# Performance work log

Measured on AMD Instinct MI355X. Metric: run time of the kernel, lower is better.

The kernel has to match this reference:

```python
import math
import jax, jax.numpy as jnp
import numpy as np

L, H, W_SIZE, EPS = 4, 4, 64, 1e-5


def _sinusoidal_pe(T, D):
    pos = np.arange(T, dtype=np.float32)[:, None]
    div = np.exp(np.arange(0, D, 2, dtype=np.float32) * -(math.log(10000.0) / D))
    pe = np.zeros((T, D), dtype=np.float32)
    pe[:, 0::2] = np.sin(pos * div)
    pe[:, 1::2] = np.cos(pos * div)
    return jnp.asarray(pe)


def _layernorm(x, g, b):
    mu = jnp.mean(x, axis=-1, keepdims=True)
    var = jnp.mean(jnp.square(x - mu), axis=-1, keepdims=True)
    return (x - mu) * jax.lax.rsqrt(var + EPS) * g + b


def setup_inputs() -> dict:
    key = jax.random.key(0)
    B, T, D, F = 4, 2048, 256, 1024
    ks = jax.random.split(key, 8)
    s = 0.02
    return {
        "tokens": jax.random.normal(ks[0], (B, T, D), jnp.float32),
        "Wqkv": jax.random.normal(ks[1], (L, 3 * D, D), jnp.float32) * s,
        "bqkv": jnp.zeros((L, 3 * D), jnp.float32),
        "Wo": jax.random.normal(ks[2], (L, D, D), jnp.float32) * s,
        "bo": jnp.zeros((L, D), jnp.float32),
        "W1": jax.random.normal(ks[3], (L, F, D), jnp.float32) * s,
        "b1": jnp.zeros((L, F), jnp.float32),
        "W2": jax.random.normal(ks[4], (L, D, F), jnp.float32) * s,
        "b2": jnp.zeros((L, D), jnp.float32),
        "ln1_g": jnp.ones((L, D), jnp.float32),
        "ln1_b": jnp.zeros((L, D), jnp.float32),
        "ln2_g": jnp.ones((L, D), jnp.float32),
        "ln2_b": jnp.zeros((L, D), jnp.float32),
        "lnf_g": jnp.ones((D,), jnp.float32),
        "lnf_b": jnp.zeros((D,), jnp.float32),
    }


def reference(tokens, Wqkv, bqkv, Wo, bo, W1, b1, W2, b2,
              ln1_g, ln1_b, ln2_g, ln2_b, lnf_g, lnf_b):
    B, T, D = tokens.shape
    hd = D // H
    x = tokens + _sinusoidal_pe(T, D)[None]  # (B,T,D)

    # sliding-window causal mask: i attends to max(0, i-W+1)..i
    idx = jnp.arange(T)
    i, j = idx[:, None], idx[None, :]
    allowed = (j <= i) & (j >= i - W_SIZE + 1)
    bias = jnp.where(allowed, 0.0, -1e9).astype(jnp.float32)  # (T,T)

    def step(x, p):
        Wqkv, bqkv, Wo, bo, W1, b1, W2, b2, g1, be1, g2, be2 = p
        x2 = _layernorm(x, g1, be1)
        qkv = x2 @ Wqkv.T + bqkv                      # (B,T,3D)
        q, k, v = jnp.split(qkv, 3, axis=-1)
        q = q.reshape(B, T, H, hd)
        k = k.reshape(B, T, H, hd)
        v = v.reshape(B, T, H, hd)
        scores = jnp.einsum("bthd,bshd->bhts", q, k) / math.sqrt(hd)
        attn = jax.nn.softmax(scores + bias, axis=-1)
        o = jnp.einsum("bhts,bshd->bthd", attn, v).reshape(B, T, D)
        x = x + o @ Wo.T + bo
        x3 = _layernorm(x, g2, be2)
        h = jax.nn.gelu(x3 @ W1.T + b1, approximate=False)
        x = x + h @ W2.T + b2
        return x, None

    x, _ = jax.lax.scan(step, x, (Wqkv, bqkv, Wo, bo, W1, b1, W2, b2,
                                  ln1_g, ln1_b, ln2_g, ln2_b))
    return _layernorm(x, lnf_g, lnf_b)
```

## Files before the change

### kernel.cpp

```cpp
#include <hip/hip_runtime.h>
#include <hip/hip_bf16.h>
#include <math.h>

#define BB 4
#define TT 2048
#define DD 256
#define FF 1024
#define NL 4

typedef __bf16 bf16x8 __attribute__((ext_vector_type(8)));
typedef float f32x4 __attribute__((ext_vector_type(4)));

__device__ __forceinline__ float gelu_f(float v) {
  float x = fabsf(v) * 0.70710678118654752f;
  float t = 1.0f / fmaf(0.3275911f, x, 1.0f);
  float p = t * fmaf(t, fmaf(t, fmaf(t, fmaf(t, 1.061405429f, -1.453152027f),
                                     1.421413741f), -0.284496736f), 0.254829592f);
  float erfv = copysignf(1.0f - p * __expf(-x * x), v);
  return 0.5f * v * (1.0f + erfv);
}

__global__ __launch_bounds__(256) void prologue_kernel(
    const float4* __restrict__ wq, const float4* __restrict__ wo,
    const float4* __restrict__ w1, const float4* __restrict__ w2,
    ushort4* __restrict__ dst,
    const float* __restrict__ tokens, const float* __restrict__ g,
    const float* __restrict__ b, float* __restrict__ x,
    __hip_bfloat16* __restrict__ sb) {
  if (blockIdx.x < 3072) {
    int gi = blockIdx.x * 256 + threadIdx.x;
    const float4* src;
    int off;
    if (gi < 196608)      { src = wq; off = gi; }
    else if (gi < 262144) { src = wo; off = gi - 196608; }
    else if (gi < 524288) { src = w1; off = gi - 262144; }
    else                  { src = w2; off = gi - 524288; }
    float4 v = src[off];
    ushort4 o;
    o.x = __hip_bfloat16_raw(__float2bfloat16(v.x)).x;
    o.y = __hip_bfloat16_raw(__float2bfloat16(v.y)).x;
    o.z = __hip_bfloat16_raw(__float2bfloat16(v.z)).x;
    o.w = __hip_bfloat16_raw(__float2bfloat16(v.w)).x;
    dst[gi] = o;
    return;
  }
  int row = (blockIdx.x - 3072) * 4 + (threadIdx.x >> 6);
  int lane = threadIdx.x & 63;
  int t = row & (TT - 1);
  const float* xr = tokens + (size_t)row * DD;
  float v[4];
  float s = 0.f;
#pragma unroll
  for (int i = 0; i < 4; ++i) {
    int d = lane + 64 * i;
    int i2 = d & ~1;
    float freq = expf((float)i2 * -(9.210340371976184f / 256.f));
    float ang = (float)t * freq;
    float pe = (d & 1) ? cosf(ang) : sinf(ang);
    v[i] = xr[d] + pe;
    s += v[i];
  }
#pragma unroll
  for (int off = 32; off; off >>= 1) s += __shfl_xor(s, off, 64);
  float mu = s * (1.f / DD);
  float vs = 0.f;
#pragma unroll
  for (int i = 0; i < 4; ++i) { float dd = v[i] - mu; vs = fmaf(dd, dd, vs); }
#pragma unroll
  for (int off = 32; off; off >>= 1) vs += __shfl_xor(vs, off, 64);
  float rr = rsqrtf(vs * (1.f / DD) + 1e-5f);
#pragma unroll
  for (int i = 0; i < 4; ++i) {
    int d = lane + 64 * i;
    x[(size_t)row * DD + d] = v[i];
    sb[(size_t)row * DD + d] = __float2bfloat16((v[i] - mu) * rr * g[d] + b[d]);
  }
}

template <int MW, int NW, int BK, int KTOT, int ACT>
__global__ __launch_bounds__(256) void mgemm_kernel(
    const __hip_bfloat16* __restrict__ A, const __hip_bfloat16* __restrict__ B,
    const float* __restrict__ bias, __hip_bfloat16* __restrict__ Cout,
    int M, int N) {
  constexpr int BM = 32 * MW, BN = 32 * NW, ROWS = BM + BN;
  constexpr int NCH = BK / 32;
  constexpr int CHB = ROWS * 32;
  constexpr int RG = ROWS / 16;
  constexpr int NST = NCH * RG;
  __shared__ __align__(16) __hip_bfloat16 sm[NCH * CHB];
  const int tid = threadIdx.x;
  const int wave = tid >> 6, lane = tid & 63;
  const int m0 = blockIdx.y * BM, n0 = blockIdx.x * BN;
  const int wm = (wave >> 1) * (16 * MW), wn = (wave & 1) * (16 * NW);
  const int quad = lane >> 4, lr = lane & 15;
  const int srow = lane >> 2, scol = (lane & 3) * 8;

  f32x4 acc[MW][NW] = {};

  for (int kt = 0; kt < KTOT; kt += BK) {
    __syncthreads();
#pragma unroll
    for (int i = 0; i < NST / 4; ++i) {
      int inst = i * 4 + wave;
      int c = inst / RG, grp = inst - c * RG;
      int r = grp * 16 + srow;
      const __hip_bfloat16* gp =
          (r < BM) ? (A + (size_t)(m0 + r) * KTOT + kt + c * 32 + scol)
                   : (B + (size_t)(n0 + (r - BM)) * KTOT + kt + c * 32 + scol);
      __builtin_amdgcn_global_load_lds(
          (const __attribute__((address_space(1))) unsigned int*)gp,
          (__attribute__((address_space(3))) unsigned int*)(sm + c * CHB + grp * 512),
          16, 0, 0);
    }
    __syncthreads();
#pragma unroll
    for (int c = 0; c < NCH; ++c) {
      bf16x8 af[MW], bfr[NW];
#pragma unroll
      for (int mi = 0; mi < MW; ++mi)
        af[mi] = *(const bf16x8*)(sm + c * CHB + (wm + mi * 16 + lr) * 32 + quad * 8);
#pragma unroll
      for (int ni = 0; ni < NW; ++ni)
        bfr[ni] = *(const bf16x8*)(sm + c * CHB + (BM + wn + ni * 16 + lr) * 32 + quad * 8);
#pragma unroll
      for (int mi = 0; mi < MW; ++mi)
#pragma unroll
        for (int ni = 0; ni < NW; ++ni)
          acc[mi][ni] = __builtin_amdgcn_mfma_f32_16x16x32_bf16(
              af[mi], bfr[ni], acc[mi][ni], 0, 0, 0);
    }
  }

#pragma unroll
  for (int mi = 0; mi < MW; ++mi) {
#pragma unroll
    for (int ni = 0; ni < NW; ++ni) {
      int col = n0 + wn + ni * 16 + lr;
      float bv = bias[col];
#pragma unroll
      for (int r = 0; r < 4; ++r) {
        int row = m0 + wm + mi * 16 + quad * 4 + r;
        float v = acc[mi][ni][r] + bv;
        if (ACT == 1) v = gelu_f(v);
        Cout[(size_t)row * N + col] = __float2bfloat16(v);
      }
    }
  }
}

template <int KTOT, int FIN>
__global__ __launch_bounds__(256) void mgemm_ln_kernel(
    const __hip_bfloat16* __restrict__ A, const __hip_bfloat16* __restrict__ B,
    const float* __restrict__ bias, const float* __restrict__ res,
    const float* __restrict__ g, const float* __restrict__ bb,
    float* __restrict__ xout, void* __restrict__ yout) {
  constexpr int BM = 32, ROWS = BM + 256;
  constexpr int BK = 64, NCH = BK / 32;
  constexpr int CHB = ROWS * 32;
  constexpr int RG = ROWS / 16;
  constexpr int NST = NCH * RG;
  __shared__ __align__(16) __hip_bfloat16 sm[NCH * CHB];
  __shared__ float red1[4][BM], red2[4][BM];
  const int tid = threadIdx.x;
  const int wave = tid >> 6, lane = tid & 63;
  const int quad = lane >> 4, lr = lane & 15;
  const int m0 = blockIdx.x * BM;
  const int srow = lane >> 2, scol = (lane & 3) * 8;

  f32x4 acc[2][4] = {};

  for (int kt = 0; kt < KTOT; kt += BK) {
    __syncthreads();
#pragma unroll
    for (int i = 0; i < NST / 4; ++i) {
      int inst = i * 4 + wave;
      int c = inst / RG, grp = inst - c * RG;
      int r = grp * 16 + srow;
      const __hip_bfloat16* gp =
          (r < BM) ? (A + (size_t)(m0 + r) * KTOT + kt + c * 32 + scol)
                   : (B + (size_t)(r - BM) * KTOT + kt + c * 32 + scol);
      __builtin_amdgcn_global_load_lds(
          (const __attribute__((address_space(1))) unsigned int*)gp,
          (__attribute__((address_space(3))) unsigned int*)(sm + c * CHB + grp * 512),
          16, 0, 0);
    }
    __syncthreads();
#pragma unroll
    for (int c = 0; c < NCH; ++c) {
      bf16x8 af[2], bfr[4];
#pragma unroll
      for (int mi = 0; mi < 2; ++mi)
        af[mi] = *(const bf16x8*)(sm + c * CHB + (mi * 16 + lr) * 32 + quad * 8);
#pragma unroll
      for (int ni = 0; ni < 4; ++ni)
        bfr[ni] = *(const bf16x8*)(sm + c * CHB + (BM + wave * 64 + ni * 16 + lr) * 32 + quad * 8);
#pragma unroll
      for (int mi = 0; mi < 2; ++mi)
#pragma unroll
        for (int ni = 0; ni < 4; ++ni)
          acc[mi][ni] = __builtin_amdgcn_mfma_f32_16x16x32_bf16(
              af[mi], bfr[ni], acc[mi][ni], 0, 0, 0);
    }
  }

  float v[2][4][4];
  float s1[2][4] = {}, s2[2][4] = {};
#pragma unroll
  for (int mi = 0; mi < 2; ++mi)
#pragma unroll
    for (int ni = 0; ni < 4; ++ni) {
      int col = wave * 64 + ni * 16 + lr;
      float bv = bias[col];
#pragma unroll
      for (int r = 0; r < 4; ++r) {
        int row = m0 + mi * 16 + quad * 4 + r;
        float val = acc[mi][ni][r] + bv + res[(size_t)row * DD + col];
        v[mi][ni][r] = val;
        s1[mi][r] += val;
        s2[mi][r] = fmaf(val, val, s2[mi][r]);
      }
    }
#pragma unroll
  for (int mi = 0; mi < 2; ++mi)
#pragma unroll
    for (int r = 0; r < 4; ++r) {
#pragma unroll
      for (int off = 8; off; off >>= 1) {
        s1[mi][r] += __shfl_xor(s1[mi][r], off, 64);
        s2[mi][r] += __shfl_xor(s2[mi][r], off, 64);
      }
    }
  if (lr == 0) {
#pragma unroll
    for (int mi = 0; mi < 2; ++mi)
#pragma unroll
      for (int r = 0; r < 4; ++r) {
        red1[wave][mi * 16 + quad * 4 + r] = s1[mi][r];
        red2[wave][mi * 16 + quad * 4 + r] = s2[mi][r];
      }
  }
  __syncthreads();
#pragma unroll
  for (int mi = 0; mi < 2; ++mi)
#pragma unroll
    for (int r = 0; r < 4; ++r) {
      int rl = mi * 16 + quad * 4 + r;
      float ssum = red1[0][rl] + red1[1][rl] + red1[2][rl] + red1[3][rl];
      float qsum = red2[0][rl] + red2[1][rl] + red2[2][rl] + red2[3][rl];
      float mu = ssum * (1.f / DD);
      float var = qsum * (1.f / DD) - mu * mu;
      float rr = rsqrtf(var + 1e-5f);
      int row = m0 + rl;
#pragma unroll
      for (int ni = 0; ni < 4; ++ni) {
        int col = wave * 64 + ni * 16 + lr;
        float y = (v[mi][ni][r] - mu) * rr * g[col] + bb[col];
        if (FIN) {
          ((float*)yout)[(size_t)row * DD + col] = y;
        } else {
          ((__hip_bfloat16*)yout)[(size_t)row * DD + col] = __float2bfloat16(y);
          xout[(size_t)row * DD + col] = v[mi][ni][r];
        }
      }
    }
}

__global__ __launch_bounds__(256) void attn_kernel(const __hip_bfloat16* __restrict__ qkv,
                                                   __hip_bfloat16* __restrict__ o) {
  __shared__ __align__(16) __hip_bfloat16 KsPs[128 * 72];
  __shared__ __align__(16) __hip_bfloat16 Vt[64 * 136];
  const int bh = blockIdx.y;
  const int b = bh >> 2, h = bh & 3;
  const int t0 = blockIdx.x * 64;
  const int sbase = t0 - 63;
  const int tid = threadIdx.x;

  const __hip_bfloat16* kb = qkv + (size_t)(b * TT) * 768 + 256 + h * 64;
  const __hip_bfloat16* vb = kb + 256;
  union U8 { uint4 u; __hip_bfloat16 hx[8]; };
#pragma unroll
  for (int it = 0; it < 4; ++it) {
    int f = tid + it * 256;
    int si = f >> 3;
    int c8 = f & 7;
    int s = sbase + si;
    U8 kr, vr;
    kr.u = make_uint4(0, 0, 0, 0); vr.u = make_uint4(0, 0, 0, 0);
    if (s >= 0 && s < TT) {
      kr.u = *(const uint4*)&kb[(size_t)s * 768 + 8 * c8];
      vr.u = *(const uint4*)&vb[(size_t)s * 768 + 8 * c8];
    }
    *(uint4*)&KsPs[si * 72 + c8 * 8] = kr.u;
    int pc = (si >> 3) ^ c8;
#pragma unroll
    for (int j = 0; j < 8; ++j) Vt[(c8 * 8 + j) * 136 + pc * 8 + (si & 7)] = vr.hx[j];
  }
  __syncthreads();

  const int wave = tid >> 6, lane = tid & 63;
  const int quad = lane >> 4, lr = lane & 15;

  const __hip_bfloat16* qrow = qkv + (size_t)(b * TT + t0 + wave * 16 + lr) * 768 + h * 64;
  bf16x8 qa0 = *(const bf16x8*)(qrow + quad * 8);
  bf16x8 qa1 = *(const bf16x8*)(qrow + 32 + quad * 8);
  f32x4 sc[8];
#pragma unroll
  for (int c = 0; c < 8; ++c) {
    f32x4 a = {};
    bf16x8 kf0 = *(const bf16x8*)&KsPs[(c * 16 + lr) * 72 + quad * 8];
    a = __builtin_amdgcn_mfma_f32_16x16x32_bf16(qa0, kf0, a, 0, 0, 0);
    bf16x8 kf1 = *(const bf16x8*)&KsPs[(c * 16 + lr) * 72 + 32 + quad * 8];
    a = __builtin_amdgcn_mfma_f32_16x16x32_bf16(qa1, kf1, a, 0, 0, 0);
    sc[c] = a;
  }
  __syncthreads();

#pragma unroll
  for (int reg = 0; reg < 4; ++reg) {
    int dt = wave * 16 + quad * 4 + reg;
    float pv[8];
    float mx = -1e30f;
#pragma unroll
    for (int c = 0; c < 8; ++c) {
      int si = c * 16 + lr;
      float v = sc[c][reg] * 0.125f;
      bool ok = (si >= dt) && (si <= dt + 63) && (sbase + si >= 0);
      v = ok ? v : -1e30f;
      pv[c] = v;
      mx = fmaxf(mx, v);
    }
#pragma unroll
    for (int off = 8; off; off >>= 1) mx = fmaxf(mx, __shfl_xor(mx, off, 64));
    float l = 0.f;
#pragma unroll
    for (int c = 0; c < 8; ++c) { float e = __expf(pv[c] - mx); pv[c] = e; l += e; }
#pragma unroll
    for (int off = 8; off; off >>= 1) l += __shfl_xor(l, off, 64);
    float rinv = 1.f / l;
#pragma unroll
    for (int c = 0; c < 8; ++c)
      KsPs[(wave * 16 + quad * 4 + reg) * 136 + c * 16 + lr] = __float2bfloat16(pv[c] * rinv);
  }

  __hip_bfloat16* obase = o + (size_t)(b * TT) * DD + h * 64;
#pragma unroll
  for (int ct = 0; ct < 4; ++ct) {
    f32x4 acc = {};
#pragma unroll
    for (int kk = 0; kk < 4; ++kk) {
      bf16x8 pa = *(const bf16x8*)&KsPs[(wave * 16 + lr) * 136 + kk * 32 + quad * 8];
      int dd = ct * 16 + lr;
      bf16x8 vf = *(const bf16x8*)&Vt[dd * 136 + (((kk * 4 + quad) ^ (dd >> 3)) * 8)];
      acc = __builtin_amdgcn_mfma_f32_16x16x32_bf16(pa, vf, acc, 0, 0, 0);
    }
#pragma unroll
    for (int reg = 0; reg < 4; ++reg) {
      int t = t0 + wave * 16 + quad * 4 + reg;
      obase[(size_t)t * DD + ct * 16 + lr] = __float2bfloat16(acc[reg]);
    }
  }
}

extern "C" void kernel_launch(void* const* d_in, const int* in_sizes, int n_in,
                              void* d_out, int out_size, void* d_ws, size_t ws_size,
                              hipStream_t stream) {
  const float* tokens = (const float*)d_in[0];
  const float* Wqkv = (const float*)d_in[1];
  const float* bqkv = (const float*)d_in[2];
  const float* Wo   = (const float*)d_in[3];
  const float* bo   = (const float*)d_in[4];
  const float* W1   = (const float*)d_in[5];
  const float* b1   = (const float*)d_in[6];
  const float* W2   = (const float*)d_in[7];
  const float* b2   = (const float*)d_in[8];
  const float* ln1g = (const float*)d_in[9];
  const float* ln1b = (const float*)d_in[10];
  const float* ln2g = (const float*)d_in[11];
  const float* ln2b = (const float*)d_in[12];
  const float* lnfg = (const float*)d_in[13];
  const float* lnfb = (const float*)d_in[14];
  float* out = (float*)d_out;

  const int M = BB * TT;
  const int ND = M * DD;

  float* x = (float*)d_ws;
  __hip_bfloat16* sb  = (__hip_bfloat16*)(x + ND);
  __hip_bfloat16* big = sb + (size_t)M * DD;
  __hip_bfloat16* wqb = big + (size_t)M * FF;
  __hip_bfloat16* wob = wqb + (size_t)NL * 3 * DD * DD;
  __hip_bfloat16* w1b = wob + (size_t)NL * DD * DD;
  __hip_bfloat16* w2b = w1b + (size_t)NL * FF * DD;

  prologue_kernel<<<3072 + M / 4, 256, 0, stream>>>(
      (const float4*)Wqkv, (const float4*)Wo, (const float4*)W1,
      (const float4*)W2, (ushort4*)wqb, tokens, ln1g, ln1b, x, sb);

  for (int l = 0; l < NL; ++l) {
    mgemm_kernel<2, 4, 64, 256, 0><<<dim3(6, 128), 256, 0, stream>>>(
        sb, wqb + (size_t)l * 768 * DD, bqkv + l * 768, big, M, 768);
    attn_kernel<<<dim3(TT / 64, BB * 4), 256, 0, stream>>>(big, sb);
    mgemm_ln_kernel<256, 0><<<M / 32, 256, 0, stream>>>(
        sb, wob + (size_t)l * DD * DD, bo + l * DD, x,
        ln2g + l * DD, ln2b + l * DD, x, sb);
    mgemm_kernel<2, 4, 64, 256, 1><<<dim3(8, 128), 256, 0, stream>>>(
        sb, w1b + (size_t)l * FF * DD, b1 + l * FF, big, M, FF);
    if (l < NL - 1) {
      mgemm_ln_kernel<1024, 0><<<M / 32, 256, 0, stream>>>(
          big, w2b + (size_t)l * DD * FF, b2 + l * DD, x,
          ln1g + (l + 1) * DD, ln1b + (l + 1) * DD, x, sb);
    } else {
      mgemm_ln_kernel<1024, 1><<<M / 32, 256, 0, stream>>>(
          big, w2b + (size_t)l * DD * FF, b2 + l * DD, x,
          lnfg, lnfb, nullptr, out);
    }
  }
}
```

Measured before the change: 371.7 us.

## Fuse FFN up/down projections, LayerNorm and next-layer QKV GEMM into one kernel

Adds an mlp_kernel in which each 32-row block computes W1+GELU in 128-wide chunks held in LDS, accumulates the W2 projection, applies residual plus LayerNorm, and then runs the next layer's QKV projection from LDS. This removes the round trip of the (M,1024) hidden activation through global memory and two kernel launches per layer. In exchange each block re-streams all weights with no cross-block reuse, using only 256 blocks with large LDS (~84KB). Occupancy is low and there is no double buffering.

Result: slower. 397.5 us (+6.9%).

```diff
diff --git a/kernel.cpp b/kernel.cpp
--- a/kernel.cpp
+++ b/kernel.cpp
@@ -10,6 +10,12 @@
 
 typedef __bf16 bf16x8 __attribute__((ext_vector_type(8)));
 typedef float f32x4 __attribute__((ext_vector_type(4)));
+
+__device__ __forceinline__ void stage16(const __hip_bfloat16* gp, __hip_bfloat16* lp) {
+  __builtin_amdgcn_global_load_lds(
+      (const __attribute__((address_space(1))) unsigned int*)gp,
+      (__attribute__((address_space(3))) unsigned int*)lp, 16, 0, 0);
+}
 
 __device__ __forceinline__ float gelu_f(float v) {
   float x = fabsf(v) * 0.70710678118654752f;
@@ -107,10 +113,7 @@
       const __hip_bfloat16* gp =
           (r < BM) ? (A + (size_t)(m0 + r) * KTOT + kt + c * 32 + scol)
                    : (B + (size_t)(n0 + (r - BM)) * KTOT + kt + c * 32 + scol);
-      __builtin_amdgcn_global_load_lds(
-          (const __attribute__((address_space(1))) unsigned int*)gp,
-          (__attribute__((address_space(3))) unsigned int*)(sm + c * CHB + grp * 512),
-          16, 0, 0);
+      stage16(gp, sm + c * CHB + grp * 512);
     }
     __syncthreads();
 #pragma unroll
@@ -179,10 +182,7 @@
       const __hip_bfloat16* gp =
           (r < BM) ? (A + (size_t)(m0 + r) * KTOT + kt + c * 32 + scol)
                    : (B + (size_t)(r - BM) * KTOT + kt + c * 32 + scol);
-      __builtin_amdgcn_global_load_lds(
-          (const __attribute__((address_space(1))) unsigned int*)gp,
-          (__attribute__((address_space(3))) unsigned int*)(sm + c * CHB + grp * 512),
-          16, 0, 0);
+      stage16(gp, sm + c * CHB + grp * 512);
     }
     __syncthreads();
 #pragma unroll
@@ -263,6 +263,221 @@
         }
       }
     }
+}
+
+template <int LAST>
+__global__ __launch_bounds__(256) void mlp_kernel(
+    const __hip_bfloat16* __restrict__ sb, const __hip_bfloat16* __restrict__ w1,
+    const float* __restrict__ b1, const __hip_bfloat16* __restrict__ w2,
+    const float* __restrict__ b2, const __hip_bfloat16* __restrict__ wq,
+    const float* __restrict__ bq, const float* __restrict__ g,
+    const float* __restrict__ bb, float* __restrict__ x,
+    __hip_bfloat16* __restrict__ big, float* __restrict__ out) {
+  __shared__ __align__(16) __hip_bfloat16 asbuf[8 * 1024];
+  __shared__ __align__(16) __hip_bfloat16 sbuf2[8 * 1024];
+  __shared__ __align__(16) __hip_bfloat16 hbuf[32 * 136];
+  __shared__ __align__(16) __hip_bfloat16 wstage[16384];
+  __shared__ float red1[4][32], red2[4][32];
+  const int tid = threadIdx.x;
+  const int wave = tid >> 6, lane = tid & 63;
+  const int quad = lane >> 4, lr = lane & 15;
+  const int srow = lane >> 2, scol = (lane & 3) * 8;
+  const int t0 = blockIdx.x * 32;
+
+#pragma unroll
+  for (int i = 0; i < 4; ++i) {
+    int inst = i * 4 + wave;
+    int c = inst >> 1, grp = inst & 1;
+    int r = grp * 16 + srow;
+    stage16(sb + (size_t)(t0 + r) * 256 + c * 32 + scol,
+            asbuf + c * 1024 + grp * 512);
+  }
+  __syncthreads();
+
+  f32x4 xacc[2][4] = {};
+  for (int fc = 0; fc < 8; ++fc) {
+    const int ff0 = fc * 128;
+    f32x4 hacc[2][2] = {};
+#pragma unroll
+    for (int kt2 = 0; kt2 < 2; ++kt2) {
+      __syncthreads();
+#pragma unroll
+      for (int i = 0; i < 8; ++i) {
+        int inst = i * 4 + wave;
+        int c2 = inst >> 3, grp = inst & 7;
+        int r = grp * 16 + srow;
+        stage16(w1 + (size_t)(ff0 + r) * 256 + kt2 * 128 + c2 * 32 + scol,
+                wstage + c2 * 4096 + grp * 512);
+      }
+      __syncthreads();
+#pragma unroll
+      for (int c2 = 0; c2 < 4; ++c2) {
+        bf16x8 af[2], bfr[2];
+#pragma unroll
+        for (int mi = 0; mi < 2; ++mi)
+          af[mi] = *(const bf16x8*)(asbuf + (kt2 * 4 + c2) * 1024 + (mi * 16 + lr) * 32 + quad * 8);
+#pragma unroll
+        for (int ni = 0; ni < 2; ++ni)
+          bfr[ni] = *(const bf16x8*)(wstage + c2 * 4096 + (wave * 2 + ni) * 512 + lr * 32 + quad * 8);
+#pragma unroll
+        for (int mi = 0; mi < 2; ++mi)
+#pragma unroll
+          for (int ni = 0; ni < 2; ++ni)
+            hacc[mi][ni] = __builtin_amdgcn_mfma_f32_16x16x32_bf16(
+                af[mi], bfr[ni], hacc[mi][ni], 0, 0, 0);
+      }
+    }
+#pragma unroll
+    for (int mi = 0; mi < 2; ++mi)
+#pragma unroll
+      for (int ni = 0; ni < 2; ++ni) {
+        int col = wave * 32 + ni * 16 + lr;
+        float bv = b1[ff0 + col];
+#pragma unroll
+        for (int r = 0; r < 4; ++r)
+          hbuf[(mi * 16 + quad * 4 + r) * 136 + col] =
+              __float2bfloat16(gelu_f(hacc[mi][ni][r] + bv));
+      }
+    __syncthreads();
+#pragma unroll
+    for (int kt3 = 0; kt3 < 2; ++kt3) {
+      if (kt3) __syncthreads();
+#pragma unroll
+      for (int i = 0; i < 8; ++i) {
+        int inst = i * 4 + wave;
+        int c2 = inst >> 4, grp = inst & 15;
+        int r = grp * 16 + srow;
+        stage16(w2 + (size_t)r * 1024 + ff0 + kt3 * 64 + c2 * 32 + scol,
+                wstage + c2 * 8192 + grp * 512);
+      }
+      __syncthreads();
+#pragma unroll
+      for (int c2 = 0; c2 < 2; ++c2) {
+        bf16x8 af[2], bfr[4];
+#pragma unroll
+        for (int mi = 0; mi < 2; ++mi)
+          af[mi] = *(const bf16x8*)(hbuf + (mi * 16 + lr) * 136 + kt3 * 64 + c2 * 32 + quad * 8);
+#pragma unroll
+        for (int ni = 0; ni < 4; ++ni)
+          bfr[ni] = *(const bf16x8*)(wstage + c2 * 8192 + (wave * 4 + ni) * 512 + lr * 32 + quad * 8);
+#pragma unroll
+        for (int mi = 0; mi < 2; ++mi)
+#pragma unroll
+          for (int ni = 0; ni < 4; ++ni)
+            xacc[mi][ni] = __builtin_amdgcn_mfma_f32_16x16x32_bf16(
+                af[mi], bfr[ni], xacc[mi][ni], 0, 0, 0);
+      }
+    }
+  }
+
+  float v[2][4][4];
+  float s1[2][4] = {}, s2[2][4] = {};
+#pragma unroll
+  for (int mi = 0; mi < 2; ++mi)
+#pragma unroll
+    for (int ni = 0; ni < 4; ++ni) {
+      int col = wave * 64 + ni * 16 + lr;
+      float bv = b2[col];
+#pragma unroll
+      for (int r = 0; r < 4; ++r) {
+        int row = t0 + mi * 16 + quad * 4 + r;
+        float val = xacc[mi][ni][r] + bv + x[(size_t)row * DD + col];
+        v[mi][ni][r] = val;
+        s1[mi][r] += val;
+        s2[mi][r] = fmaf(val, val, s2[mi][r]);
+      }
+    }
+#pragma unroll
+  for (int mi = 0; mi < 2; ++mi)
+#pragma unroll
+    for (int r = 0; r < 4; ++r) {
+#pragma unroll
+      for (int off = 8; off; off >>= 1) {
+        s1[mi][r] += __shfl_xor(s1[mi][r], off, 64);
+        s2[mi][r] += __shfl_xor(s2[mi][r], off, 64);
+      }
+    }
+  if (lr == 0) {
+#pragma unroll
+    for (int mi = 0; mi < 2; ++mi)
+#pragma unroll
+      for (int r = 0; r < 4; ++r) {
+        red1[wave][mi * 16 + quad * 4 + r] = s1[mi][r];
+        red2[wave][mi * 16 + quad * 4 + r] = s2[mi][r];
+      }
+  }
+  __syncthreads();
+#pragma unroll
+  for (int mi = 0; mi < 2; ++mi)
+#pragma unroll
+    for (int r = 0; r < 4; ++r) {
+      int rl = mi * 16 + quad * 4 + r;
+      float ssum = red1[0][rl] + red1[1][rl] + red1[2][rl] + red1[3][rl];
+      float qsum = red2[0][rl] + red2[1][rl] + red2[2][rl] + red2[3][rl];
+      float mu = ssum * (1.f / DD);
+      float var = qsum * (1.f / DD) - mu * mu;
+      float rr = rsqrtf(var + 1e-5f);
+      int row = t0 + rl;
+#pragma unroll
+      for (int ni = 0; ni < 4; ++ni) {
+        int col = wave * 64 + ni * 16 + lr;
+        float y = (v[mi][ni][r] - mu) * rr * g[col] + bb[col];
+        if (LAST) {
+          out[(size_t)row * DD + col] = y;
+        } else {
+          x[(size_t)row * DD + col] = v[mi][ni][r];
+          sbuf2[(col >> 5) * 1024 + rl * 32 + (col & 31)] = __float2bfloat16(y);
+        }
+      }
+    }
+
+  if (!LAST) {
+    __syncthreads();
+    for (int nc = 0; nc < 6; ++nc) {
+      f32x4 qacc[2][2] = {};
+#pragma unroll
+      for (int kt2 = 0; kt2 < 2; ++kt2) {
+        __syncthreads();
+#pragma unroll
+        for (int i = 0; i < 8; ++i) {
+          int inst = i * 4 + wave;
+          int c2 = inst >> 3, grp = inst & 7;
+          int r = grp * 16 + srow;
+          stage16(wq + (size_t)(nc * 128 + r) * 256 + kt2 * 128 + c2 * 32 + scol,
+                  wstage + c2 * 4096 + grp * 512);
+        }
+        __syncthreads();
+#pragma unroll
+        for (int c2 = 0; c2 < 4; ++c2) {
+          bf16x8 af[2], bfr[2];
+#pragma unroll
+          for (int mi = 0; mi < 2; ++mi)
+            af[mi] = *(const bf16x8*)(sbuf2 + (kt2 * 4 + c2) * 1024 + (mi * 16 + lr) * 32 + quad * 8);
+#pragma unroll
+          for (int ni = 0; ni < 2; ++ni)
+            bfr[ni] = *(const bf16x8*)(wstage + c2 * 4096 + (wave * 2 + ni) * 512 + lr * 32 + quad * 8);
+#pragma unroll
+          for (int mi = 0; mi < 2; ++mi)
+#pragma unroll
+            for (int ni = 0; ni < 2; ++ni)
+              qacc[mi][ni] = __builtin_amdgcn_mfma_f32_16x16x32_bf16(
+                  af[mi], bfr[ni], qacc[mi][ni], 0, 0, 0);
+        }
+      }
+#pragma unroll
+      for (int mi = 0; mi < 2; ++mi)
+#pragma unroll
+        for (int ni = 0; ni < 2; ++ni) {
+          int col = nc * 128 + wave * 32 + ni * 16 + lr;
+          float bv = bq[col];
+#pragma unroll
+          for (int r = 0; r < 4; ++r) {
+            int row = t0 + mi * 16 + quad * 4 + r;
+            big[(size_t)row * 768 + col] = __float2bfloat16(qacc[mi][ni][r] + bv);
+          }
+        }
+    }
+  }
 }
 
 __global__ __launch_bounds__(256) void attn_kernel(const __hip_bfloat16* __restrict__ qkv,
@@ -396,23 +611,25 @@
       (const float4*)Wqkv, (const float4*)Wo, (const float4*)W1,
       (const float4*)W2, (ushort4*)wqb, tokens, ln1g, ln1b, x, sb);
 
+  mgemm_kernel<2, 4, 64, 256, 0><<<dim3(6, 128), 256, 0, stream>>>(
+      sb, wqb, bqkv, big, M, 768);
+
   for (int l = 0; l < NL; ++l) {
-    mgemm_kernel<2, 4, 64, 256, 0><<<dim3(6, 128), 256, 0, stream>>>(
-        sb, wqb + (size_t)l * 768 * DD, bqkv + l * 768, big, M, 768);
     attn_kernel<<<dim3(TT / 64, BB * 4), 256, 0, stream>>>(big, sb);
     mgemm_ln_kernel<256, 0><<<M / 32, 256, 0, stream>>>(
         sb, wob + (size_t)l * DD * DD, bo + l * DD, x,
         ln2g + l * DD, ln2b + l * DD, x, sb);
-    mgemm_kernel<2, 4, 64, 256, 1><<<dim3(8, 128), 256, 0, stream>>>(
-        sb, w1b + (size_t)l * FF * DD, b1 + l * FF, big, M, FF);
     if (l < NL - 1) {
-      mgemm_ln_kernel<1024, 0><<<M / 32, 256, 0, stream>>>(
-          big, w2b + (size_t)l * DD * FF, b2 + l * DD, x,
-          ln1g + (l + 1) * DD, ln1b + (l + 1) * DD, x, sb);
+      mlp_kernel<0><<<M / 32, 256, 0, stream>>>(
+          sb, w1b + (size_t)l * FF * DD, b1 + l * FF,
+          w2b + (size_t)l * DD * FF, b2 + l * DD,
+          wqb + (size_t)(l + 1) * 768 * DD, bqkv + (l + 1) * 768,
+          ln1g + (l + 1) * DD, ln1b + (l + 1) * DD, x, big, nullptr);
     } else {
-      mgemm_ln_kernel<1024, 1><<<M / 32, 256, 0, stream>>>(
-          big, w2b + (size_t)l * DD * FF, b2 + l * DD, x,
-          lnfg, lnfb, nullptr, out);
-    }
-  }
-}
+      mlp_kernel<1><<<M / 32, 256, 0, stream>>>(
+          sb, w1b + (size_t)l * FF * DD, b1 + l * FF,
+          w2b + (size_t)l * DD * FF, b2 + l * DD,
+          nullptr, nullptr, lnfg, lnfb, x, nullptr, out);
+    }
+  }
+}
```

## Split W2 GEMM from fused residual-LayerNorm into tiled GEMM plus row-LN kernel

Applied to the files above, without the earlier changes.

The FFN down-projection (K=1024) no longer uses the fused GEMM+LayerNorm kernel with 32-row blocks spanning all 256 columns. It now runs as a regular tiled GEMM with 64x64 tiles and fp32 output into a new workspace buffer, followed by a separate residual-add plus LayerNorm kernel. This gives 512 blocks instead of 256 and smaller per-block B tiles, which is meant to improve occupancy and load balance for the heaviest GEMM. The cost is an extra fp32 round trip through global memory and one more launch per layer. The QKV GEMM launch is also reordered so it follows the new LN kernel.

New measurement: 361.1 us. 2.8% less time.

```diff
diff --git a/kernel.cpp b/kernel.cpp
--- a/kernel.cpp
+++ b/kernel.cpp
@@ -10,6 +10,12 @@
 
 typedef __bf16 bf16x8 __attribute__((ext_vector_type(8)));
 typedef float f32x4 __attribute__((ext_vector_type(4)));
+
+__device__ __forceinline__ void stage16(const __hip_bfloat16* gp, __hip_bfloat16* lp) {
+  __builtin_amdgcn_global_load_lds(
+      (const __attribute__((address_space(1))) unsigned int*)gp,
+      (__attribute__((address_space(3))) unsigned int*)lp, 16, 0, 0);
+}
 
 __device__ __forceinline__ float gelu_f(float v) {
   float x = fabsf(v) * 0.70710678118654752f;
@@ -77,10 +83,10 @@
   }
 }
 
-template <int MW, int NW, int BK, int KTOT, int ACT>
+template <int MW, int NW, int BK, int KTOT, int ACT, int OUTF>
 __global__ __launch_bounds__(256) void mgemm_kernel(
     const __hip_bfloat16* __restrict__ A, const __hip_bfloat16* __restrict__ B,
-    const float* __restrict__ bias, __hip_bfloat16* __restrict__ Cout,
+    const float* __restrict__ bias, void* __restrict__ Cout,
     int M, int N) {
   constexpr int BM = 32 * MW, BN = 32 * NW, ROWS = BM + BN;
   constexpr int NCH = BK / 32;
@@ -107,10 +113,7 @@
       const __hip_bfloat16* gp =
           (r < BM) ? (A + (size_t)(m0 + r) * KTOT + kt + c * 32 + scol)
                    : (B + (size_t)(n0 + (r - BM)) * KTOT + kt + c * 32 + scol);
-      __builtin_amdgcn_global_load_lds(
-          (const __attribute__((address_space(1))) unsigned int*)gp,
-          (__attribute__((address_space(3))) unsigned int*)(sm + c * CHB + grp * 512),
-          16, 0, 0);
+      stage16(gp, sm + c * CHB + grp * 512);
     }
     __syncthreads();
 #pragma unroll
@@ -142,18 +145,19 @@
         int row = m0 + wm + mi * 16 + quad * 4 + r;
         float v = acc[mi][ni][r] + bv;
         if (ACT == 1) v = gelu_f(v);
-        Cout[(size_t)row * N + col] = __float2bfloat16(v);
+        if (OUTF) ((float*)Cout)[(size_t)row * N + col] = v;
+        else ((__hip_bfloat16*)Cout)[(size_t)row * N + col] = __float2bfloat16(v);
       }
     }
   }
 }
 
-template <int KTOT, int FIN>
+template <int KTOT>
 __global__ __launch_bounds__(256) void mgemm_ln_kernel(
     const __hip_bfloat16* __restrict__ A, const __hip_bfloat16* __restrict__ B,
     const float* __restrict__ bias, const float* __restrict__ res,
     const float* __restrict__ g, const float* __restrict__ bb,
-    float* __restrict__ xout, void* __restrict__ yout) {
+    float* __restrict__ xout, __hip_bfloat16* __restrict__ yout) {
   constexpr int BM = 32, ROWS = BM + 256;
   constexpr int BK = 64, NCH = BK / 32;
   constexpr int CHB = ROWS * 32;
@@ -179,10 +183,7 @@
       const __hip_bfloat16* gp =
           (r < BM) ? (A + (size_t)(m0 + r) * KTOT + kt + c * 32 + scol)
                    : (B + (size_t)(r - BM) * KTOT + kt + c * 32 + scol);
-      __builtin_amdgcn_global_load_lds(
-          (const __attribute__((address_space(1))) unsigned int*)gp,
-          (__attribute__((address_space(3))) unsigned int*)(sm + c * CHB + grp * 512),
-          16, 0, 0);
+      stage16(gp, sm + c * CHB + grp * 512);
     }
     __syncthreads();
 #pragma unroll
@@ -255,14 +256,50 @@
       for (int ni = 0; ni < 4; ++ni) {
         int col = wave * 64 + ni * 16 + lr;
         float y = (v[mi][ni][r] - mu) * rr * g[col] + bb[col];
-        if (FIN) {
-          ((float*)yout)[(size_t)row * DD + col] = y;
-        } else {
-          ((__hip_bfloat16*)yout)[(size_t)row * DD + col] = __float2bfloat16(y);
-          xout[(size_t)row * DD + col] = v[mi][ni][r];
-        }
+        yout[(size_t)row * DD + col] = __float2bfloat16(y);
+        xout[(size_t)row * DD + col] = v[mi][ni][r];
       }
     }
+}
+
+template <int FIN>
+__global__ __launch_bounds__(256) void rln_kernel(
+    const float* __restrict__ go, const float* __restrict__ xin,
+    const float* __restrict__ g, const float* __restrict__ b,
+    float* __restrict__ xout, __hip_bfloat16* __restrict__ sbout,
+    float* __restrict__ out) {
+  int row = blockIdx.x * 4 + (threadIdx.x >> 6);
+  int lane = threadIdx.x & 63;
+  const float* gr = go + (size_t)row * DD;
+  const float* xr = xin + (size_t)row * DD;
+  float v[4];
+  float s = 0.f;
+#pragma unroll
+  for (int i = 0; i < 4; ++i) {
+    int d = lane + 64 * i;
+    v[i] = gr[d] + xr[d];
+    s += v[i];
+  }
+#pragma unroll
+  for (int off = 32; off; off >>= 1) s += __shfl_xor(s, off, 64);
+  float mu = s * (1.f / DD);
+  float vs = 0.f;
+#pragma unroll
+  for (int i = 0; i < 4; ++i) { float dd = v[i] - mu; vs = fmaf(dd, dd, vs); }
+#pragma unroll
+  for (int off = 32; off; off >>= 1) vs += __shfl_xor(vs, off, 64);
+  float rr = rsqrtf(vs * (1.f / DD) + 1e-5f);
+#pragma unroll
+  for (int i = 0; i < 4; ++i) {
+    int d = lane + 64 * i;
+    float y = (v[i] - mu) * rr * g[d] + b[d];
+    if (FIN) {
+      out[(size_t)row * DD + d] = y;
+    } else {
+      xout[(size_t)row * DD + d] = v[i];
+      sbout[(size_t)row * DD + d] = __float2bfloat16(y);
+    }
+  }
 }
 
 __global__ __launch_bounds__(256) void attn_kernel(const __hip_bfloat16* __restrict__ qkv,
@@ -391,28 +428,32 @@
   __hip_bfloat16* wob = wqb + (size_t)NL * 3 * DD * DD;
   __hip_bfloat16* w1b = wob + (size_t)NL * DD * DD;
   __hip_bfloat16* w2b = w1b + (size_t)NL * FF * DD;
+  float* gbuf = (float*)(w2b + (size_t)NL * DD * FF);
 
   prologue_kernel<<<3072 + M / 4, 256, 0, stream>>>(
       (const float4*)Wqkv, (const float4*)Wo, (const float4*)W1,
       (const float4*)W2, (ushort4*)wqb, tokens, ln1g, ln1b, x, sb);
 
+  mgemm_kernel<2, 4, 64, 256, 0, 0><<<dim3(6, 128), 256, 0, stream>>>(
+      sb, wqb, bqkv, big, M, 768);
+
   for (int l = 0; l < NL; ++l) {
-    mgemm_kernel<2, 4, 64, 256, 0><<<dim3(6, 128), 256, 0, stream>>>(
-        sb, wqb + (size_t)l * 768 * DD, bqkv + l * 768, big, M, 768);
     attn_kernel<<<dim3(TT / 64, BB * 4), 256, 0, stream>>>(big, sb);
-    mgemm_ln_kernel<256, 0><<<M / 32, 256, 0, stream>>>(
+    mgemm_ln_kernel<256><<<M / 32, 256, 0, stream>>>(
         sb, wob + (size_t)l * DD * DD, bo + l * DD, x,
         ln2g + l * DD, ln2b + l * DD, x, sb);
-    mgemm_kernel<2, 4, 64, 256, 1><<<dim3(8, 128), 256, 0, stream>>>(
+    mgemm_kernel<2, 4, 64, 256, 1, 0><<<dim3(8, 128), 256, 0, stream>>>(
         sb, w1b + (size_t)l * FF * DD, b1 + l * FF, big, M, FF);
+    mgemm_kernel<2, 2, 64, 1024, 0, 1><<<dim3(4, 128), 256, 0, stream>>>(
+        big, w2b + (size_t)l * DD * FF, b2 + l * DD, gbuf, M, DD);
     if (l < NL - 1) {
-      mgemm_ln_kernel<1024, 0><<<M / 32, 256, 0, stream>>>(
-          big, w2b + (size_t)l * DD * FF, b2 + l * DD, x,
-          ln1g + (l + 1) * DD, ln1b + (l + 1) * DD, x, sb);
+      rln_kernel<0><<<M / 4, 256, 0, stream>>>(
+          gbuf, x, ln1g + (l + 1) * DD, ln1b + (l + 1) * DD, x, sb, nullptr);
+      mgemm_kernel<2, 4, 64, 256, 0, 0><<<dim3(6, 128), 256, 0, stream>>>(
+          sb, wqb + (size_t)(l + 1) * 768 * DD, bqkv + (l + 1) * 768, big, M, 768);
     } else {
-      mgemm_ln_kernel<1024, 1><<<M / 32, 256, 0, stream>>>(
-          big, w2b + (size_t)l * DD * FF, b2 + l * DD, x,
-          lnfg, lnfb, nullptr, out);
-    }
-  }
-}
+      rln_kernel<1><<<M / 4, 256, 0, stream>>>(
+          gbuf, x, lnfg, lnfb, nullptr, nullptr, out);
+    }
+  }
+}
```
